# Kernel optimization log

Measured on AMD Instinct MI355X. Metric: run time of the kernel, lower is better.

The kernel has to match this reference:

```python
import jax, jax.numpy as jnp
import numpy as np

N = 50000      # nodes across the batched graph
E = 400000     # edges
F_IN = 128     # gnn_input_size
H = 3          # num_head
D = 64         # gnn_hidden_size
G = 64         # graphs in batch
P = 64         # pattern_input_size
NEG_GAT = 0.2  # GATv2Conv leaky_relu slope (dgl default)
NEG = 0.01     # nn.LeakyReLU default slope


def setup_inputs() -> dict:
    key = jax.random.key(0)
    ks = jax.random.split(key, 32)
    rn = lambda k, s, sc=0.05: jax.random.normal(k, s, dtype=jnp.float32) * sc
    HD = H * D
    return {
        "inputs": rn(ks[0], (N, F_IN), 1.0),
        "src": jax.random.randint(ks[1], (E,), 0, N),
        "dst": jax.random.randint(ks[2], (E,), 0, N),
        "graph_ids": jnp.sort(jax.random.randint(ks[3], (N,), 0, G)),
        "p1": rn(ks[4], (G, P), 1.0),
        "p2": rn(ks[5], (G, P), 1.0),
        "p3": rn(ks[6], (G, P), 1.0),
        # GATv2 layer params: fc_src, fc_dst, attn vector, bias
        "W1s": rn(ks[7], (F_IN, HD)), "W1d": rn(ks[8], (F_IN, HD)),
        "a1": rn(ks[9], (H, D)), "b1": rn(ks[10], (HD,)),
        "W2s": rn(ks[11], (HD, HD)), "W2d": rn(ks[12], (HD, HD)),
        "a2": rn(ks[13], (H, D)), "b2": rn(ks[14], (HD,)),
        "W3s": rn(ks[15], (HD, HD)), "W3d": rn(ks[16], (HD, HD)),
        "a3": rn(ks[17], (H, D)), "b3": rn(ks[18], (HD,)),
        # pattern branch (forward only uses ex_layer1 for all three inputs)
        "Wex": rn(ks[19], (P, 32)), "bex": rn(ks[20], (32,)),
        "Wpat": rn(ks[21], (96, P)), "bpat": rn(ks[22], (P,)),
        # classifier head
        "Wc1": rn(ks[23], (D + P, 64)), "bc1": rn(ks[24], (64,)),
        "Wc2": rn(ks[25], (64, 32)), "bc2": rn(ks[26], (32,)),
        "Wc3": rn(ks[27], (32, 2)), "bc3": rn(ks[28], (2,)),
    }


def _gatv2(x, src, dst, Ws, Wd, attn, bias):
    # dgl GATv2Conv (share_weights=False): e = a . leaky_relu(Ws x_u + Wd x_v)
    fs = (x @ Ws).reshape(N, H, D)
    fd = (x @ Wd).reshape(N, H, D)
    e = jax.nn.leaky_relu(fs[src] + fd[dst], NEG_GAT)            # [E,H,D]
    logits = jnp.einsum('ehd,hd->eh', e, attn)                   # [E,H]
    m = jax.ops.segment_max(logits, dst, num_segments=N)         # [N,H]
    m = jnp.where(jnp.isfinite(m), m, 0.0)                       # nodes w/o in-edges
    ex = jnp.exp(logits - m[dst])
    denom = jax.ops.segment_sum(ex, dst, num_segments=N)         # [N,H]
    alpha = ex / jnp.maximum(denom, 1e-9)[dst]                   # edge softmax
    out = jax.ops.segment_sum(alpha[:, :, None] * fs[src], dst, num_segments=N)
    return out + bias.reshape(1, H, D)                           # [N,H,D]


def reference(inputs, src, dst, graph_ids, p1, p2, p3,
              W1s, W1d, a1, b1, W2s, W2d, a2, b2, W3s, W3d, a3, b3,
              Wex, bex, Wpat, bpat, Wc1, bc1, Wc2, bc2, Wc3, bc3):
    h = _gatv2(inputs, src, dst, W1s, W1d, a1, b1).reshape(N, H * D)
    h = _gatv2(h, src, dst, W2s, W2d, a2, b2).reshape(N, H * D)
    h = _gatv2(h, src, dst, W3s, W3d, a3, b3).mean(axis=1)       # [N,D]
    # dgl.mean_nodes: per-graph mean over nodes
    sums = jax.ops.segment_sum(h, graph_ids, num_segments=G)
    cnts = jax.ops.segment_sum(jnp.ones((N,), h.dtype), graph_ids, num_segments=G)
    gnn_out = sums / jnp.maximum(cnts, 1.0)[:, None]             # [G,D]
    # pattern branch (ex_layer1 applied to all three, as in source)
    px = jnp.concatenate([p1 @ Wex + bex, p2 @ Wex + bex, p3 @ Wex + bex], axis=1)
    px = jax.nn.leaky_relu(px @ Wpat + bpat, NEG)                # [G,P]
    x = jnp.concatenate([gnn_out, px], axis=1)                   # [G,D+P]
    x = jax.nn.leaky_relu(x @ Wc1 + bc1, NEG)
    x = jax.nn.leaky_relu(x @ Wc2 + bc2, NEG)
    return x @ Wc3 + bc3                                         # [G,2]
```

## Files before the change

### kernel.cpp

```cpp
#include <hip/hip_runtime.h>
#include <cstdint>
#include <cstddef>

#define NN 50000
#define EE 400000
#define FIN 128
#define HH 3
#define DD 64
#define GG 64
#define PP 64
#define HD 192

typedef short bf16x8 __attribute__((ext_vector_type(8)));
typedef float f32x4 __attribute__((ext_vector_type(4)));
typedef unsigned int u32x2 __attribute__((ext_vector_type(2)));

__device__ inline int wsumi(int v) {
#pragma unroll
    for (int m = 32; m > 0; m >>= 1) v += __shfl_xor(v, m, 64);
    return v;
}

__device__ inline float bf2f(unsigned short u) {
    union { unsigned int i; float f; } x; x.i = ((unsigned int)u) << 16; return x.f;
}
__device__ inline unsigned short f2bf(float f) {
    union { float f; unsigned int i; } x; x.f = f;
    unsigned int r = x.i + 0x7FFFu + ((x.i >> 16) & 1u);
    return (unsigned short)(r >> 16);
}

__device__ inline void unp2(unsigned int w, float& lo, float& hi) {
    union { unsigned int i; float f; } x;
    x.i = w << 16;          lo = x.f;
    x.i = w & 0xFFFF0000u;  hi = x.f;
}
__device__ inline void load4(const unsigned short* p, float* o) {
    u32x2 w = *(const u32x2*)p;
    unp2(w[0], o[0], o[1]);
    unp2(w[1], o[2], o[3]);
}

__global__ void k_count(const int* __restrict__ dst, int* __restrict__ counts) {
    int e = blockIdx.x * 256 + threadIdx.x;
    if (e < EE) atomicAdd(&counts[dst[e]], 1);
}

__global__ void k_scan_block(const int* __restrict__ in, int* __restrict__ out,
                             int* __restrict__ bsums) {
    __shared__ int tmp[1024];
    int tid = threadIdx.x;
    int i = blockIdx.x * 1024 + tid;
    int v = (i < NN) ? in[i] : 0;
    tmp[tid] = v;
    __syncthreads();
    for (int off = 1; off < 1024; off <<= 1) {
        int t = (tid >= off) ? tmp[tid - off] : 0;
        __syncthreads();
        tmp[tid] += t;
        __syncthreads();
    }
    if (i < NN) out[i] = tmp[tid] - v;
    if (tid == 1023) bsums[blockIdx.x] = tmp[1023];
}

__global__ void k_scan_add(int* __restrict__ row_ptr, const int* __restrict__ bsums, int nb) {
    __shared__ int sbase;
    int tid = threadIdx.x;
    if (tid < 64) {
        int v = (tid < blockIdx.x) ? bsums[tid] : 0;
        v = wsumi(v);
        if (tid == 0) sbase = v;
    }
    __syncthreads();
    int i = blockIdx.x * 1024 + tid;
    if (i < NN) row_ptr[i] += sbase;
    else if (i == NN) row_ptr[NN] = EE;
}

__global__ void k_scatter(const int* __restrict__ src, const int* __restrict__ dst,
                          const int* __restrict__ row_ptr, int* __restrict__ cursor,
                          int* __restrict__ csr_src) {
    int e = blockIdx.x * 256 + threadIdx.x;
    if (e >= EE) return;
    int v = dst[e];
    int pos = row_ptr[v] + atomicAdd(&cursor[v], 1);
    csr_src[pos] = src[e];
}

__device__ inline void pack_one(const float* __restrict__ W, unsigned short* __restrict__ WP,
                                int id, int Kc) {
    int lane = id & 63;
    int kc = (id >> 6) % Kc;
    int ct = (id >> 6) / Kc;
    int n = ct * 16 + (lane & 15);
    int kb = kc * 32 + (lane >> 4) * 8;
#pragma unroll
    for (int j = 0; j < 8; j++)
        WP[(unsigned)id * 8 + j] = f2bf(W[(unsigned)(kb + j) * HD + n]);
}

#define IDS128 (12 * 4 * 64)
#define IDS192 (12 * 6 * 64)
__global__ void k_pack_all(const float* W1s, const float* W1d,
                           const float* W2s, const float* W2d,
                           const float* W3s, const float* W3d,
                           unsigned short* P1s, unsigned short* P1d,
                           unsigned short* P2s, unsigned short* P2d,
                           unsigned short* P3s, unsigned short* P3d) {
    int idx = blockIdx.x * 256 + threadIdx.x;
    if (idx < IDS128) { pack_one(W1s, P1s, idx, 4); return; }
    idx -= IDS128;
    if (idx < IDS128) { pack_one(W1d, P1d, idx, 4); return; }
    idx -= IDS128;
    if (idx < IDS192) { pack_one(W2s, P2s, idx, 6); return; }
    idx -= IDS192;
    if (idx < IDS192) { pack_one(W2d, P2d, idx, 6); return; }
    idx -= IDS192;
    if (idx < IDS192) { pack_one(W3s, P3s, idx, 6); return; }
    idx -= IDS192;
    if (idx < IDS192) { pack_one(W3d, P3d, idx, 6); return; }
}

template <int K, bool BF16IN>
__global__ __launch_bounds__(256) void k_gemm_mfma(const void* __restrict__ Xin,
                                                   const unsigned short* __restrict__ WPs,
                                                   const unsigned short* __restrict__ WPd,
                                                   unsigned short* __restrict__ FS,
                                                   unsigned short* __restrict__ FD) {
    constexpr int Kc = K / 32;
    __shared__ unsigned short xs[16][K + 8];
    __shared__ unsigned short cs[16][392];
    int tid = threadIdx.x;
    int row0 = blockIdx.x * 16;
    if (BF16IN) {
        const unsigned short* XB = (const unsigned short*)Xin;
        for (int c = tid; c < 16 * K / 8; c += 256) {
            int r = c / (K / 8), kk = (c - r * (K / 8)) * 8;
            *(bf16x8*)&xs[r][kk] = *(const bf16x8*)&XB[(unsigned)((row0 + r) * K + kk)];
        }
    } else {
        const float* X = (const float*)Xin;
        for (int idx = tid; idx < 16 * K; idx += 256) {
            int r = idx / K, k = idx - r * K;
            xs[r][k] = f2bf(X[(unsigned)((row0 + r) * K + k)]);
        }
    }
    __syncthreads();

    int lane = tid & 63, wv = tid >> 6;
    int m = lane & 15, quad = lane >> 4;
    f32x4 acc[6];
#pragma unroll
    for (int t = 0; t < 6; t++) acc[t] = (f32x4){0.f, 0.f, 0.f, 0.f};

    for (int kc = 0; kc < Kc; kc++) {
        bf16x8 a = *(const bf16x8*)&xs[m][kc * 32 + quad * 8];
#pragma unroll
        for (int t = 0; t < 6; t++) {
            int ct = wv * 6 + t;
            const unsigned short* wp = (ct < 12) ? WPs : WPd;
            int c = (ct < 12) ? ct : ct - 12;
            bf16x8 b = *(const bf16x8*)&wp[(unsigned)(((c * Kc + kc) * 64 + lane) * 8)];
            acc[t] = __builtin_amdgcn_mfma_f32_16x16x32_bf16(a, b, acc[t], 0, 0, 0);
        }
    }
#pragma unroll
    for (int t = 0; t < 6; t++) {
        int ct = wv * 6 + t;
#pragma unroll
        for (int r = 0; r < 4; r++)
            cs[quad * 4 + r][ct * 16 + m] = f2bf(acc[t][r]);
    }
    __syncthreads();
#pragma unroll
    for (int it = 0; it < 3; it++) {
        int c = tid + it * 256;
        int hm = c / 384;
        int cc = c - hm * 384;
        int row = cc / 24, ch = cc - row * 24;
        unsigned short* OUT = hm ? FD : FS;
        *(bf16x8*)&OUT[(unsigned)((row0 + row) * HD + ch * 8)] =
            *(const bf16x8*)&cs[row][hm * 192 + ch * 8];
    }
}

template <bool FINAL>
__global__ __launch_bounds__(256) void k_node_gat(const int* __restrict__ row_ptr,
                                                  const int* __restrict__ csr_src,
                                                  const unsigned short* __restrict__ FS,
                                                  const unsigned short* __restrict__ FD,
                                                  const float* __restrict__ A,
                                                  const float* __restrict__ Bv,
                                                  unsigned short* __restrict__ XB,
                                                  float* __restrict__ H64) {
    int tid = threadIdx.x;
    int grp = tid >> 4, sub = tid & 15;
    int node = blockIdx.x * 16 + grp;
    int col = sub * 4;

    float a[3][4], b[3][4];
#pragma unroll
    for (int h = 0; h < 3; h++) {
        f32x4 av = *(const f32x4*)&A[h * 64 + col];
        f32x4 bv = *(const f32x4*)&Bv[h * 64 + col];
#pragma unroll
        for (int j = 0; j < 4; j++) { a[h][j] = av[j]; b[h][j] = bv[j]; }
    }

    int lo = row_ptr[node], hi = row_ptr[node + 1];

    float g[3][4];
#pragma unroll
    for (int h = 0; h < 3; h++) load4(&FD[(size_t)node * HD + h * 64 + col], g[h]);

    float r[3][4];
#pragma unroll
    for (int h = 0; h < 3; h++)
#pragma unroll
        for (int j = 0; j < 4; j++) r[h][j] = 0.f;
    float d0 = 0.f, d1 = 0.f, d2 = 0.f;

    for (int e = lo; e < hi; ++e) {
        int u = csr_src[e];
        size_t bu = (size_t)u * HD;
        float f[3][4];
#pragma unroll
        for (int h = 0; h < 3; h++) load4(&FS[bu + h * 64 + col], f[h]);

        float p0 = 0.f, p1 = 0.f, p2 = 0.f;
#pragma unroll
        for (int j = 0; j < 4; j++) {
            float s0 = f[0][j] + g[0][j]; s0 = fmaxf(s0, 0.2f * s0); p0 += s0 * a[0][j];
            float s1 = f[1][j] + g[1][j]; s1 = fmaxf(s1, 0.2f * s1); p1 += s1 * a[1][j];
            float s2 = f[2][j] + g[2][j]; s2 = fmaxf(s2, 0.2f * s2); p2 += s2 * a[2][j];
        }
#pragma unroll
        for (int m = 8; m > 0; m >>= 1) {
            p0 += __shfl_xor(p0, m, 64);
            p1 += __shfl_xor(p1, m, 64);
            p2 += __shfl_xor(p2, m, 64);
        }
        float w0 = __expf(p0), w1 = __expf(p1), w2 = __expf(p2);
#pragma unroll
        for (int j = 0; j < 4; j++) {
            r[0][j] += w0 * f[0][j];
            r[1][j] += w1 * f[1][j];
            r[2][j] += w2 * f[2][j];
        }
        d0 += w0; d1 += w1; d2 += w2;
    }

    float q0 = fmaxf(d0, 1e-9f), q1 = fmaxf(d1, 1e-9f), q2 = fmaxf(d2, 1e-9f);
    if (FINAL) {
        f32x4 m;
#pragma unroll
        for (int j = 0; j < 4; j++)
            m[j] = (r[0][j] / q0 + b[0][j] + r[1][j] / q1 + b[1][j] +
                    r[2][j] / q2 + b[2][j]) * (1.f / 3.f);
        *(f32x4*)&H64[(size_t)node * 64 + col] = m;
    } else {
        float qq[3] = {q0, q1, q2};
#pragma unroll
        for (int h = 0; h < 3; h++) {
            unsigned short o0 = f2bf(r[h][0] / qq[h] + b[h][0]);
            unsigned short o1 = f2bf(r[h][1] / qq[h] + b[h][1]);
            unsigned short o2 = f2bf(r[h][2] / qq[h] + b[h][2]);
            unsigned short o3 = f2bf(r[h][3] / qq[h] + b[h][3]);
            u32x2 w;
            w[0] = (unsigned)o0 | ((unsigned)o1 << 16);
            w[1] = (unsigned)o2 | ((unsigned)o3 << 16);
            *(u32x2*)&XB[(size_t)node * HD + h * 64 + col] = w;
        }
    }
}

__global__ __launch_bounds__(256) void k_graph_mean(const float* __restrict__ H64,
                                                    const int* __restrict__ gids,
                                                    float* __restrict__ gsum,
                                                    int* __restrict__ gcnt) {
    int g = blockIdx.x >> 2, q = blockIdx.x & 3;
    int lo, hi;
    {
        int a = 0, b = NN;
        while (a < b) { int m = (a + b) >> 1; if (gids[m] < g) a = m + 1; else b = m; }
        lo = a;
        b = NN;
        while (a < b) { int m = (a + b) >> 1; if (gids[m] < g + 1) a = m + 1; else b = m; }
        hi = a;
    }
    int len = hi - lo;
    int qlen = (len + 3) >> 2;
    int s = lo + q * qlen;
    int e = s + qlen; if (e > hi) e = hi;
    int lane = threadIdx.x & 63, wv = threadIdx.x >> 6;

    float acc = 0.f;
    for (int v = s + wv; v < e; v += 4)
        acc += H64[(size_t)v * 64 + lane];
    __shared__ float red[4][64];
    red[wv][lane] = acc;
    __syncthreads();
    if (wv == 0) {
        float t = red[0][lane] + red[1][lane] + red[2][lane] + red[3][lane];
        if (e > s) {
            atomicAdd(&gsum[g * 64 + lane], t);
            if (lane == 0) atomicAdd(&gcnt[g], e - s);
        }
    }
}

__global__ __launch_bounds__(128) void k_head(const float* __restrict__ gsum, const int* __restrict__ gcnt,
                                              const float* __restrict__ p1, const float* __restrict__ p2,
                                              const float* __restrict__ p3,
                                              const float* __restrict__ Wex, const float* __restrict__ bex,
                                              const float* __restrict__ Wpat, const float* __restrict__ bpat,
                                              const float* __restrict__ Wc1, const float* __restrict__ bc1,
                                              const float* __restrict__ Wc2, const float* __restrict__ bc2,
                                              const float* __restrict__ Wc3, const float* __restrict__ bc3,
                                              float* __restrict__ out) {
    int g = blockIdx.x;
    int tid = threadIdx.x;
    __shared__ float pbuf[192];
    __shared__ float ex[96], xc[128], t1[64], t2[32];

    if (tid < 64)       pbuf[tid] = p1[g * 64 + tid];
    else if (tid < 128) pbuf[tid] = p2[g * 64 + tid - 64];
    if (tid < 64)       pbuf[128 + tid] = p3[g * 64 + tid];
    if (tid >= 64 && tid < 128)
        xc[tid - 64] = gsum[g * 64 + tid - 64] / fmaxf((float)gcnt[g], 1.f);
    __syncthreads();
    if (tid < 96) {
        int jj = tid & 31;
        const float* pp = &pbuf[(tid >> 5) * 64];
        float acc = bex[jj];
        for (int k = 0; k < 64; k++) acc += pp[k] * Wex[k * 32 + jj];
        ex[tid] = acc;
    }
    __syncthreads();
    if (tid < 64) {
        float acc = bpat[tid];
        for (int k = 0; k < 96; k++) acc += ex[k] * Wpat[k * 64 + tid];
        xc[64 + tid] = acc > 0.f ? acc : 0.01f * acc;
    }
    __syncthreads();
    if (tid < 64) {
        float acc = bc1[tid];
        for (int k = 0; k < 128; k++) acc += xc[k] * Wc1[k * 64 + tid];
        t1[tid] = acc > 0.f ? acc : 0.01f * acc;
    }
    __syncthreads();
    if (tid < 32) {
        float acc = bc2[tid];
        for (int k = 0; k < 64; k++) acc += t1[k] * Wc2[k * 32 + tid];
        t2[tid] = acc > 0.f ? acc : 0.01f * acc;
    }
    __syncthreads();
    if (tid < 2) {
        float acc = bc3[tid];
        for (int k = 0; k < 32; k++) acc += t2[k] * Wc3[k * 2 + tid];
        out[g * 2 + tid] = acc;
    }
}

extern "C" void kernel_launch(void* const* d_in, const int* in_sizes, int n_in,
                              void* d_out, int out_size, void* d_ws, size_t ws_size,
                              hipStream_t stream) {
    const float* X0  = (const float*)d_in[0];
    const int*   src = (const int*)d_in[1];
    const int*   dst = (const int*)d_in[2];
    const int*   gid = (const int*)d_in[3];
    const float* p1  = (const float*)d_in[4];
    const float* p2  = (const float*)d_in[5];
    const float* p3  = (const float*)d_in[6];
    const float* W1s = (const float*)d_in[7],  *W1d = (const float*)d_in[8];
    const float* a1  = (const float*)d_in[9],  *b1  = (const float*)d_in[10];
    const float* W2s = (const float*)d_in[11], *W2d = (const float*)d_in[12];
    const float* a2  = (const float*)d_in[13], *b2  = (const float*)d_in[14];
    const float* W3s = (const float*)d_in[15], *W3d = (const float*)d_in[16];
    const float* a3  = (const float*)d_in[17], *b3  = (const float*)d_in[18];
    const float* Wex = (const float*)d_in[19], *bex = (const float*)d_in[20];
    const float* Wpat= (const float*)d_in[21], *bpat= (const float*)d_in[22];
    const float* Wc1 = (const float*)d_in[23], *bc1 = (const float*)d_in[24];
    const float* Wc2 = (const float*)d_in[25], *bc2 = (const float*)d_in[26];
    const float* Wc3 = (const float*)d_in[27], *bc3 = (const float*)d_in[28];
    float* out = (float*)d_out;

    char* ws = (char*)d_ws;
    size_t off = 0;
    auto alloc = [&](size_t bytes) -> char* {
        char* p = ws + off;
        off = (off + bytes + 255) & ~(size_t)255;
        return p;
    };
    unsigned short* FS = (unsigned short*)alloc((size_t)NN * HD * 2);
    unsigned short* FD = (unsigned short*)alloc((size_t)NN * HD * 2);
    unsigned short* XB = (unsigned short*)alloc((size_t)NN * HD * 2);
    float*          H64= (float*)alloc((size_t)NN * 64 * 4);
    unsigned short* P1s = (unsigned short*)alloc((size_t)192 * 192 * 2);
    unsigned short* P1d = (unsigned short*)alloc((size_t)192 * 192 * 2);
    unsigned short* P2s = (unsigned short*)alloc((size_t)192 * 192 * 2);
    unsigned short* P2d = (unsigned short*)alloc((size_t)192 * 192 * 2);
    unsigned short* P3s = (unsigned short*)alloc((size_t)192 * 192 * 2);
    unsigned short* P3d = (unsigned short*)alloc((size_t)192 * 192 * 2);
    int* row_ptr = (int*)alloc((size_t)(NN + 1) * 4);
    int* csr_src = (int*)alloc((size_t)EE * 4);
    int* bsums   = (int*)alloc(64 * 4);
    char* zbase = ws + off;
    int*   counts = (int*)alloc((size_t)NN * 4);
    int*   cursor = (int*)alloc((size_t)NN * 4);
    float* gsum   = (float*)alloc((size_t)GG * 64 * 4);
    int*   gcnt   = (int*)alloc((size_t)GG * 4);
    size_t zbytes = (size_t)((ws + off) - zbase);

    hipMemsetAsync(zbase, 0, zbytes, stream);

    int ebl = (EE + 255) / 256;
    int nb  = (NN + 1023) / 1024;
    k_count<<<ebl, 256, 0, stream>>>(dst, counts);
    k_scan_block<<<nb, 1024, 0, stream>>>(counts, row_ptr, bsums);
    k_scan_add<<<nb, 1024, 0, stream>>>(row_ptr, bsums, nb);
    k_scatter<<<ebl, 256, 0, stream>>>(src, dst, row_ptr, cursor, csr_src);
    {
        int total = 2 * IDS128 + 4 * IDS192;
        k_pack_all<<<(total + 255) / 256, 256, 0, stream>>>(W1s, W1d, W2s, W2d, W3s, W3d,
                                                            P1s, P1d, P2s, P2d, P3s, P3d);
    }

    int gblk = NN / 16;
    int nblk = NN / 16;

    k_gemm_mfma<128, false><<<gblk, 256, 0, stream>>>(X0, P1s, P1d, FS, FD);
    k_node_gat<false><<<nblk, 256, 0, stream>>>(row_ptr, csr_src, FS, FD, a1, b1, XB, nullptr);
    k_gemm_mfma<192, true><<<gblk, 256, 0, stream>>>(XB, P2s, P2d, FS, FD);
    k_node_gat<false><<<nblk, 256, 0, stream>>>(row_ptr, csr_src, FS, FD, a2, b2, XB, nullptr);
    k_gemm_mfma<192, true><<<gblk, 256, 0, stream>>>(XB, P3s, P3d, FS, FD);
    k_node_gat<true><<<nblk, 256, 0, stream>>>(row_ptr, csr_src, FS, FD, a3, b3, nullptr, H64);

    k_graph_mean<<<GG * 4, 256, 0, stream>>>(H64, gid, gsum, gcnt);
    k_head<<<GG, 128, 0, stream>>>(gsum, gcnt, p1, p2, p3, Wex, bex, Wpat, bpat,
                                   Wc1, bc1, Wc2, bc2, Wc3, bc3, out);
}
```

Before: 426.1 us.

## Split each node's in-edges across four lane groups in GAT aggregation

```diff
diff --git a/kernel.cpp b/kernel.cpp
--- a/kernel.cpp
+++ b/kernel.cpp
@@ -195,8 +195,9 @@
                                                   unsigned short* __restrict__ XB,
                                                   float* __restrict__ H64) {
     int tid = threadIdx.x;
-    int grp = tid >> 4, sub = tid & 15;
-    int node = blockIdx.x * 16 + grp;
+    int wv = tid >> 6, lane = tid & 63;
+    int grp = lane >> 4, sub = lane & 15;
+    int node = blockIdx.x * 4 + wv;
     int col = sub * 4;
 
     float a[3][4], b[3][4];
@@ -221,7 +222,7 @@
         for (int j = 0; j < 4; j++) r[h][j] = 0.f;
     float d0 = 0.f, d1 = 0.f, d2 = 0.f;
 
-    for (int e = lo; e < hi; ++e) {
+    for (int e = lo + grp; e < hi; e += 4) {
         int u = csr_src[e];
         size_t bu = (size_t)u * HD;
         float f[3][4];
@@ -251,26 +252,40 @@
         d0 += w0; d1 += w1; d2 += w2;
     }
 
+#pragma unroll
+    for (int m = 16; m <= 32; m <<= 1) {
+#pragma unroll
+        for (int h = 0; h < 3; h++)
+#pragma unroll
+            for (int j = 0; j < 4; j++) r[h][j] += __shfl_xor(r[h][j], m, 64);
+        d0 += __shfl_xor(d0, m, 64);
+        d1 += __shfl_xor(d1, m, 64);
+        d2 += __shfl_xor(d2, m, 64);
+    }
+
     float q0 = fmaxf(d0, 1e-9f), q1 = fmaxf(d1, 1e-9f), q2 = fmaxf(d2, 1e-9f);
     if (FINAL) {
-        f32x4 m;
-#pragma unroll
-        for (int j = 0; j < 4; j++)
-            m[j] = (r[0][j] / q0 + b[0][j] + r[1][j] / q1 + b[1][j] +
-                    r[2][j] / q2 + b[2][j]) * (1.f / 3.f);
-        *(f32x4*)&H64[(size_t)node * 64 + col] = m;
+        if (grp == 0) {
+            f32x4 m;
+#pragma unroll
+            for (int j = 0; j < 4; j++)
+                m[j] = (r[0][j] / q0 + b[0][j] + r[1][j] / q1 + b[1][j] +
+                        r[2][j] / q2 + b[2][j]) * (1.f / 3.f);
+            *(f32x4*)&H64[(size_t)node * 64 + col] = m;
+        }
     } else {
-        float qq[3] = {q0, q1, q2};
-#pragma unroll
-        for (int h = 0; h < 3; h++) {
-            unsigned short o0 = f2bf(r[h][0] / qq[h] + b[h][0]);
-            unsigned short o1 = f2bf(r[h][1] / qq[h] + b[h][1]);
-            unsigned short o2 = f2bf(r[h][2] / qq[h] + b[h][2]);
-            unsigned short o3 = f2bf(r[h][3] / qq[h] + b[h][3]);
+        if (grp < 3) {
+            float qq = grp == 0 ? q0 : (grp == 1 ? q1 : q2);
+            float* rh = r[grp];
+            float* bh = b[grp];
+            unsigned short o0 = f2bf(rh[0] / qq + bh[0]);
+            unsigned short o1 = f2bf(rh[1] / qq + bh[1]);
+            unsigned short o2 = f2bf(rh[2] / qq + bh[2]);
+            unsigned short o3 = f2bf(rh[3] / qq + bh[3]);
             u32x2 w;
             w[0] = (unsigned)o0 | ((unsigned)o1 << 16);
             w[1] = (unsigned)o2 | ((unsigned)o3 << 16);
-            *(u32x2*)&XB[(size_t)node * HD + h * 64 + col] = w;
+            *(u32x2*)&XB[(size_t)node * HD + grp * 64 + col] = w;
         }
     }
 }
@@ -428,7 +443,7 @@
     }
 
     int gblk = NN / 16;
-    int nblk = NN / 16;
+    int nblk = NN / 4;
 
     k_gemm_mfma<128, false><<<gblk, 256, 0, stream>>>(X0, P1s, P1d, FS, FD);
     k_node_gat<false><<<nblk, 256, 0, stream>>>(row_ptr, csr_src, FS, FD, a1, b1, XB, nullptr);
```

Measured after the change: 460.1 us. 8.0% more time.
